# Performance work log

Hardware: AMD Instinct MI355X
Metric: run time of the kernel (lower is better)

## Reference

```python
import jax, jax.numpy as jnp
import numpy as np

B, L, H = 8, 2048, 1024
MASK_IDENTITY = True


def setup_inputs() -> dict:
    key = jax.random.key(0)
    ks = jax.random.split(key, 7)
    s = 1.0 / np.sqrt(H)
    return {
        "x": jax.random.normal(ks[0], (B, L, H), dtype=jnp.float32),
        "Wq": jax.random.uniform(ks[1], (H, H), jnp.float32, -s, s),
        "bq": jax.random.uniform(ks[2], (H,), jnp.float32, -s, s),
        "Wk": jax.random.uniform(ks[3], (H, H), jnp.float32, -s, s),
        "bk": jax.random.uniform(ks[4], (H,), jnp.float32, -s, s),
        "Wv": jax.random.uniform(ks[5], (H, H), jnp.float32, -s, s),
        "bv": jax.random.uniform(ks[6], (H,), jnp.float32, -s, s),
    }


def reference(x, Wq, bq, Wk, bk, Wv, bv):
    # Linear layers (torch Linear: y = x @ W.T + b)
    q = jnp.einsum("blh,oh->blo", x, Wq) + bq
    k = jnp.einsum("blh,oh->blo", x, Wk) + bk
    v = jnp.einsum("blh,oh->blo", x, Wv) + bv
    hidden = q.shape[-1]
    # NOTE: original scales by hidden_size, not sqrt(hidden_size)
    attn = jnp.einsum("blh,bmh->blm", q / hidden, k)  # [B, L, L]
    if MASK_IDENTITY:
        mask_value = -jnp.finfo(attn.dtype).max
        eye = jnp.eye(attn.shape[-1], dtype=bool)  # [L, L]
        attn = jnp.where(eye[None, :, :], mask_value, attn)
    attn = jax.nn.softmax(attn, axis=-1)
    return jnp.einsum("blm,bmh->blh", attn, v)
```

## Files before the change

### kernel.cpp

```cpp
#include <hip/hip_runtime.h>


typedef unsigned short u16;
typedef __bf16 bfx8 __attribute__((ext_vector_type(8)));
typedef float f32x4 __attribute__((ext_vector_type(4)));

__device__ __forceinline__ u16 f2bf(float f) {
    unsigned int x = __float_as_uint(f);
    unsigned int r = (x + 0x7fffu + ((x >> 16) & 1u)) >> 16;
    return (u16)r;
}
__device__ __forceinline__ float bf2f(u16 u) {
    return __uint_as_float(((unsigned int)u) << 16);
}

__global__ void f32_to_bf16(const float* __restrict__ src, u16* __restrict__ dst, int n8) {
    int i = blockIdx.x * blockDim.x + threadIdx.x;
    if (i < n8) {
        float4 a = ((const float4*)src)[i * 2];
        float4 b = ((const float4*)src)[i * 2 + 1];
        ushort4 lo; lo.x = f2bf(a.x); lo.y = f2bf(a.y); lo.z = f2bf(a.z); lo.w = f2bf(a.w);
        ushort4 hi; hi.x = f2bf(b.x); hi.y = f2bf(b.y); hi.z = f2bf(b.z); hi.w = f2bf(b.w);
        ((ushort4*)dst)[i * 2] = lo;
        ((ushort4*)dst)[i * 2 + 1] = hi;
    }
}

__global__ void transpose_bf16(const u16* __restrict__ src, u16* __restrict__ dst) {
    __shared__ u16 s[64][64 + 8];
    int z = blockIdx.z;
    int tm = blockIdx.x * 64;
    int th = blockIdx.y * 64;
    const u16* sp = src + (long)z * 2048 * 1024;
    u16* dp = dst + (long)z * 1024 * 2048;
    int t = threadIdx.x;
#pragma unroll
    for (int p = 0; p < 4; ++p) {
        int r = p * 16 + (t >> 4);
        int c = (t & 15) * 4;
        ushort4 v = *(const ushort4*)(sp + (long)(tm + r) * 1024 + th + c);
        s[r][c] = v.x; s[r][c + 1] = v.y; s[r][c + 2] = v.z; s[r][c + 3] = v.w;
    }
    __syncthreads();
#pragma unroll
    for (int p = 0; p < 4; ++p) {
        int hr = p * 16 + (t >> 4);
        int c = (t & 15) * 4;
        ushort4 v;
        v.x = s[c][hr]; v.y = s[c + 1][hr]; v.z = s[c + 2][hr]; v.w = s[c + 3][hr];
        *(ushort4*)(dp + (long)(th + hr) * 2048 + tm + c) = v;
    }
}

__global__ void row_sum(const u16* __restrict__ P, float* __restrict__ denom) {
    int row = blockIdx.x;
    int t = threadIdx.x;
    const u16* p = P + (long)row * 2048 + t * 8;
    ushort4 a = *(const ushort4*)p;
    ushort4 b = *(const ushort4*)(p + 4);
    float s = bf2f(a.x) + bf2f(a.y) + bf2f(a.z) + bf2f(a.w)
            + bf2f(b.x) + bf2f(b.y) + bf2f(b.z) + bf2f(b.w);
#pragma unroll
    for (int off = 32; off >= 1; off >>= 1) s += __shfl_down(s, off);
    __shared__ float ws[4];
    if ((t & 63) == 0) ws[t >> 6] = s;
    __syncthreads();
    if (t == 0) denom[row] = ws[0] + ws[1] + ws[2] + ws[3];
}

#define BM 128
#define BN 128
#define BK 64

template <int MODE>
__global__ __launch_bounds__(256, 2) void gemm_nt(
    const u16* __restrict__ Ab, const u16* __restrict__ Bb,
    int K, int lda, int ldb,
    long strideA, long strideB,
    const float* __restrict__ biasCat,
    u16* __restrict__ outBf, long strideP,
    const float* __restrict__ denom,
    float* __restrict__ outF)
{
    __shared__ __align__(16) u16 sA[2][BM * BK];
    __shared__ __align__(16) u16 sB[2][BN * BK];
    const int tid  = threadIdx.x;
    const int lane = tid & 63;
    const int wid  = tid >> 6;
    const int wr = wid >> 1, wc = wid & 1;
    const int z = blockIdx.z;
    const u16* A = Ab + (long)z * strideA + (long)blockIdx.x * BM * lda;
    const u16* B = Bb + (long)z * strideB + (long)blockIdx.y * BN * ldb;
    const int ldab = lda * 2, ldbb = ldb * 2;

    f32x4 acc[4][4] = {};
    const int nt = K / BK;

    auto stage = [&](int buf, int t) {
        const char* ga = (const char*)A + (long)t * (BK * 2);
        const char* gb = (const char*)B + (long)t * (BK * 2);
#pragma unroll
        for (int i = 0; i < 4; ++i) {
            int c  = i * 256 + tid;
            int r  = c >> 3;
            int lb = (c & 7) << 4;
            int sb = lb ^ ((r & 7) << 4);
            {
                const char* g = ga + (long)r * ldab + sb;
                char* l = (char*)&sA[buf][0] + (wid << 10) + (i << 12);
                __builtin_amdgcn_global_load_lds((__attribute__((address_space(1))) void*)g,
                                                 (__attribute__((address_space(3))) void*)l, 16, 0, 0);
            }
            {
                const char* g = gb + (long)r * ldbb + sb;
                char* l = (char*)&sB[buf][0] + (wid << 10) + (i << 12);
                __builtin_amdgcn_global_load_lds((__attribute__((address_space(1))) void*)g,
                                                 (__attribute__((address_space(3))) void*)l, 16, 0, 0);
            }
        }
    };

    stage(0, 0);
    __syncthreads();
    int cur = 0;
    for (int t = 0; t < nt; ++t) {
        if (t + 1 < nt) stage(cur ^ 1, t + 1);
#pragma unroll
        for (int kk = 0; kk < 2; ++kk) {
            bfx8 av[4], bv[4];
#pragma unroll
            for (int mi = 0; mi < 4; ++mi) {
                int row = wr * 64 + mi * 16 + (lane & 15);
                int kb  = kk * 64 + ((lane >> 4) << 4);
                int off = row * 128 + (kb ^ ((row & 7) << 4));
                av[mi] = *(const bfx8*)((const char*)&sA[cur][0] + off);
            }
#pragma unroll
            for (int ni = 0; ni < 4; ++ni) {
                int row = wc * 64 + ni * 16 + (lane & 15);
                int kb  = kk * 64 + ((lane >> 4) << 4);
                int off = row * 128 + (kb ^ ((row & 7) << 4));
                bv[ni] = *(const bfx8*)((const char*)&sB[cur][0] + off);
            }
#pragma unroll
            for (int mi = 0; mi < 4; ++mi)
#pragma unroll
                for (int ni = 0; ni < 4; ++ni)
                    acc[mi][ni] = __builtin_amdgcn_mfma_f32_16x16x32_bf16(av[mi], bv[ni], acc[mi][ni], 0, 0, 0);
        }
        __syncthreads();
        cur ^= 1;
    }

#pragma unroll
    for (int mi = 0; mi < 4; ++mi) {
#pragma unroll
        for (int ni = 0; ni < 4; ++ni) {
#pragma unroll
            for (int r = 0; r < 4; ++r) {
                int grow = blockIdx.x * BM + wr * 64 + mi * 16 + ((lane >> 4) << 2) + r;
                int gcol = blockIdx.y * BN + wc * 64 + ni * 16 + (lane & 15);
                float v = acc[mi][ni][r];
                if constexpr (MODE == 0) {
                    v += biasCat[gcol];
                    if (gcol < 1024) v *= (1.0f / 1024.0f);
                    int which = gcol >> 10;
                    long dst = (long)which * (16384L * 1024) + (long)grow * 1024 + (gcol & 1023);
                    outBf[dst] = f2bf(v);
                } else if constexpr (MODE == 1) {
                    float p = (grow == gcol) ? 0.0f : __expf(v);
                    outBf[(long)z * strideP + (long)grow * 2048 + gcol] = f2bf(p);
                } else {
                    float d = denom[z * 2048 + grow];
                    outF[(long)z * (2048L * 1024) + (long)grow * 1024 + gcol] = v / d;
                }
            }
        }
    }
}

extern "C" void kernel_launch(void* const* d_in, const int* in_sizes, int n_in,
                              void* d_out, int out_size, void* d_ws, size_t ws_size,
                              hipStream_t stream) {
    const float* x  = (const float*)d_in[0];
    const float* Wq = (const float*)d_in[1];
    const float* bq = (const float*)d_in[2];
    const float* Wk = (const float*)d_in[3];
    const float* bk = (const float*)d_in[4];
    const float* Wv = (const float*)d_in[5];
    const float* bv = (const float*)d_in[6];
    float* out = (float*)d_out;

    const long XB_OFF   = 0;
    const long WB_OFF   = 33554432;
    const long BIAS_OFF = WB_OFF + 6291456;
    const long DEN_OFF  = BIAS_OFF + 12288;
    const long QKV_OFF  = DEN_OFF + 65536;
    const long PB_OFF   = QKV_OFF + 2L * 33554432;
    const unsigned long long NEED = (unsigned long long)(PB_OFF + 67108864);
    if (ws_size < NEED) return;

    char* ws = (char*)d_ws;
    u16*   xb      = (u16*)(ws + XB_OFF);
    u16*   vT      = (u16*)(ws + XB_OFF);
    u16*   Wb      = (u16*)(ws + WB_OFF);
    float* biasCat = (float*)(ws + BIAS_OFF);
    float* den     = (float*)(ws + DEN_OFF);
    u16*   qkv     = (u16*)(ws + QKV_OFF);
    u16*   qb = qkv;
    u16*   kb = qkv + 16384L * 1024;
    u16*   vb = qkv + 2L * 16384 * 1024;
    u16*   Pb = (u16*)(ws + PB_OFF);

    f32_to_bf16<<<8192, 256, 0, stream>>>(x, xb, 2097152);
    f32_to_bf16<<<512, 256, 0, stream>>>(Wq, Wb, 131072);
    f32_to_bf16<<<512, 256, 0, stream>>>(Wk, Wb + 1048576, 131072);
    f32_to_bf16<<<512, 256, 0, stream>>>(Wv, Wb + 2097152, 131072);
    hipMemcpyAsync(biasCat,        bq, 4096, hipMemcpyDeviceToDevice, stream);
    hipMemcpyAsync(biasCat + 1024, bk, 4096, hipMemcpyDeviceToDevice, stream);
    hipMemcpyAsync(biasCat + 2048, bv, 4096, hipMemcpyDeviceToDevice, stream);

    gemm_nt<0><<<dim3(128, 24, 1), 256, 0, stream>>>(
        xb, Wb, 1024, 1024, 1024, 0, 0, biasCat, qkv, 0, nullptr, nullptr);

    transpose_bf16<<<dim3(32, 16, 8), 256, 0, stream>>>(vb, vT);

    gemm_nt<1><<<dim3(16, 16, 8), 256, 0, stream>>>(
        qb, kb, 1024, 1024, 1024, 2048L * 1024, 2048L * 1024,
        nullptr, Pb, 2048L * 2048, nullptr, nullptr);

    row_sum<<<16384, 256, 0, stream>>>(Pb, den);

    gemm_nt<2><<<dim3(16, 8, 8), 256, 0, stream>>>(
        Pb, vT, 2048, 2048, 2048, 2048L * 2048, 1024L * 2048,
        nullptr, nullptr, 0, den, out);
}
```

Baseline: 437.5 us.

## Use 256x256 8-wave GEMM with phased pipeline and fuse row sums

Replaces the 128x128 4-wave GEMM with a 256x256 tile, 512-thread kernel. The new kernel uses a four-phase main loop that interleaves LDS reads, global-to-LDS prefetch up to two k-steps ahead, barriers and setprio around MFMA clusters. The softmax denominator is now accumulated in the QK^T epilogue through shuffle reduction and atomicAdd, which removes the separate row_sum pass over P and needs a memset of den. The larger tiles raise data reuse but cut block counts (e.g. 256 blocks for the PV GEMM) and use 128KB LDS, which risks occupancy and SM fill.

```diff
diff --git a/kernel.cpp b/kernel.cpp
--- a/kernel.cpp
+++ b/kernel.cpp
@@ -52,128 +52,139 @@
     }
 }
 
-__global__ void row_sum(const u16* __restrict__ P, float* __restrict__ denom) {
-    int row = blockIdx.x;
-    int t = threadIdx.x;
-    const u16* p = P + (long)row * 2048 + t * 8;
-    ushort4 a = *(const ushort4*)p;
-    ushort4 b = *(const ushort4*)(p + 4);
-    float s = bf2f(a.x) + bf2f(a.y) + bf2f(a.z) + bf2f(a.w)
-            + bf2f(b.x) + bf2f(b.y) + bf2f(b.z) + bf2f(b.w);
-#pragma unroll
-    for (int off = 32; off >= 1; off >>= 1) s += __shfl_down(s, off);
-    __shared__ float ws[4];
-    if ((t & 63) == 0) ws[t >> 6] = s;
-    __syncthreads();
-    if (t == 0) denom[row] = ws[0] + ws[1] + ws[2] + ws[3];
-}
-
-#define BM 128
-#define BN 128
-#define BK 64
+
+#define PH_MID() do{ asm volatile("" ::: "memory"); __builtin_amdgcn_s_barrier(); \
+    asm volatile("s_waitcnt lgkmcnt(0)" ::: "memory"); __builtin_amdgcn_sched_barrier(0); \
+    __builtin_amdgcn_s_setprio(1); }while(0)
+#define PH_END() do{ __builtin_amdgcn_s_setprio(0); asm volatile("" ::: "memory"); \
+    __builtin_amdgcn_s_barrier(); }while(0)
+
+#define RD_A(cur, mibase) do{ \
+    const char* _b = smem + (cur)*65536 + (wr*128 + (mibase)*16 + rA)*128; \
+    a[0][0] = *(const bfx8*)(_b + 0*2048 + ofk0); a[0][1] = *(const bfx8*)(_b + 0*2048 + ofk1); \
+    a[1][0] = *(const bfx8*)(_b + 1*2048 + ofk0); a[1][1] = *(const bfx8*)(_b + 1*2048 + ofk1); \
+    a[2][0] = *(const bfx8*)(_b + 2*2048 + ofk0); a[2][1] = *(const bfx8*)(_b + 2*2048 + ofk1); \
+    a[3][0] = *(const bfx8*)(_b + 3*2048 + ofk0); a[3][1] = *(const bfx8*)(_b + 3*2048 + ofk1); \
+}while(0)
+
+#define RD_B(cur, nibase) do{ \
+    const char* _b = smem + (cur)*65536 + 32768 + (wc*64 + (nibase)*16 + rA)*128; \
+    b[(nibase)+0][0] = *(const bfx8*)(_b + 0*2048 + ofk0); b[(nibase)+0][1] = *(const bfx8*)(_b + 0*2048 + ofk1); \
+    b[(nibase)+1][0] = *(const bfx8*)(_b + 1*2048 + ofk0); b[(nibase)+1][1] = *(const bfx8*)(_b + 1*2048 + ofk1); \
+}while(0)
+
+#define MMQ(M0, N0) do{ \
+    _Pragma("unroll") \
+    for (int ks = 0; ks < 2; ++ks) \
+    _Pragma("unroll") \
+    for (int mi = 0; mi < 4; ++mi) \
+    _Pragma("unroll") \
+    for (int ni = 0; ni < 2; ++ni) \
+        acc[(M0)+mi][(N0)+ni] = __builtin_amdgcn_mfma_f32_16x16x32_bf16(a[mi][ks], b[(N0)+ni][ks], acc[(M0)+mi][(N0)+ni], 0, 0, 0); \
+}while(0)
 
 template <int MODE>
-__global__ __launch_bounds__(256, 2) void gemm_nt(
+__global__ __launch_bounds__(512, 2) void gemm8(
     const u16* __restrict__ Ab, const u16* __restrict__ Bb,
     int K, int lda, int ldb,
     long strideA, long strideB,
     const float* __restrict__ biasCat,
     u16* __restrict__ outBf, long strideP,
-    const float* __restrict__ denom,
+    float* __restrict__ den,
     float* __restrict__ outF)
 {
-    __shared__ __align__(16) u16 sA[2][BM * BK];
-    __shared__ __align__(16) u16 sB[2][BN * BK];
+    __shared__ __align__(16) char smem[131072];
     const int tid  = threadIdx.x;
     const int lane = tid & 63;
     const int wid  = tid >> 6;
-    const int wr = wid >> 1, wc = wid & 1;
+    const int wr = wid >> 2, wc = wid & 3;
     const int z = blockIdx.z;
-    const u16* A = Ab + (long)z * strideA + (long)blockIdx.x * BM * lda;
-    const u16* B = Bb + (long)z * strideB + (long)blockIdx.y * BN * ldb;
-    const int ldab = lda * 2, ldbb = ldb * 2;
-
-    f32x4 acc[4][4] = {};
-    const int nt = K / BK;
-
-    auto stage = [&](int buf, int t) {
-        const char* ga = (const char*)A + (long)t * (BK * 2);
-        const char* gb = (const char*)B + (long)t * (BK * 2);
-#pragma unroll
-        for (int i = 0; i < 4; ++i) {
-            int c  = i * 256 + tid;
-            int r  = c >> 3;
-            int lb = (c & 7) << 4;
-            int sb = lb ^ ((r & 7) << 4);
-            {
-                const char* g = ga + (long)r * ldab + sb;
-                char* l = (char*)&sA[buf][0] + (wid << 10) + (i << 12);
-                __builtin_amdgcn_global_load_lds((__attribute__((address_space(1))) void*)g,
-                                                 (__attribute__((address_space(3))) void*)l, 16, 0, 0);
-            }
-            {
-                const char* g = gb + (long)r * ldbb + sb;
-                char* l = (char*)&sB[buf][0] + (wid << 10) + (i << 12);
-                __builtin_amdgcn_global_load_lds((__attribute__((address_space(1))) void*)g,
-                                                 (__attribute__((address_space(3))) void*)l, 16, 0, 0);
-            }
+    const u16* A = Ab + (long)z * strideA + (long)blockIdx.x * 256 * lda;
+    const u16* B = Bb + (long)z * strideB + (long)blockIdx.y * 256 * ldb;
+    const int NT = K >> 6;
+
+    const int rA  = lane & 15;
+    const int cg  = lane >> 4;
+    const int swz = rA & 7;
+    const int ofk0 = ((cg)     ^ swz) << 4;
+    const int ofk1 = ((cg | 4) ^ swz) << 4;
+
+    f32x4 acc[8][4] = {};
+    bfx8 a[4][2], b[4][2];
+
+    auto stage = [&](int buf, int isB, int half, int t) {
+        const u16* src = isB ? B : A;
+        const int ld = isB ? ldb : lda;
+#pragma unroll
+        for (int rnd = 0; rnd < 2; ++rnd) {
+            int c = rnd * 512 + tid;
+            int row = half * 128 + (c >> 3);
+            int slot = c & 7;
+            const u16* g = src + (long)row * ld + t * 64 + ((slot ^ (row & 7)) << 3);
+            char* l = (char*)smem + buf * 65536 + isB * 32768 + half * 16384 + rnd * 8192 + wid * 1024;
+            __builtin_amdgcn_global_load_lds((__attribute__((address_space(1))) void*)g,
+                                             (__attribute__((address_space(3))) void*)l, 16, 0, 0);
         }
     };
 
-    stage(0, 0);
-    __syncthreads();
+    stage(0, 0, 0, 0); stage(0, 0, 1, 0); stage(0, 1, 0, 0); stage(0, 1, 1, 0);
+    stage(1, 1, 0, 1); stage(1, 1, 1, 1);
+    asm volatile("s_waitcnt vmcnt(4)" ::: "memory");
+    __builtin_amdgcn_s_barrier();
+
     int cur = 0;
-    for (int t = 0; t < nt; ++t) {
-        if (t + 1 < nt) stage(cur ^ 1, t + 1);
-#pragma unroll
-        for (int kk = 0; kk < 2; ++kk) {
-            bfx8 av[4], bv[4];
-#pragma unroll
-            for (int mi = 0; mi < 4; ++mi) {
-                int row = wr * 64 + mi * 16 + (lane & 15);
-                int kb  = kk * 64 + ((lane >> 4) << 4);
-                int off = row * 128 + (kb ^ ((row & 7) << 4));
-                av[mi] = *(const bfx8*)((const char*)&sA[cur][0] + off);
-            }
-#pragma unroll
-            for (int ni = 0; ni < 4; ++ni) {
-                int row = wc * 64 + ni * 16 + (lane & 15);
-                int kb  = kk * 64 + ((lane >> 4) << 4);
-                int off = row * 128 + (kb ^ ((row & 7) << 4));
-                bv[ni] = *(const bfx8*)((const char*)&sB[cur][0] + off);
-            }
-#pragma unroll
-            for (int mi = 0; mi < 4; ++mi)
-#pragma unroll
-                for (int ni = 0; ni < 4; ++ni)
-                    acc[mi][ni] = __builtin_amdgcn_mfma_f32_16x16x32_bf16(av[mi], bv[ni], acc[mi][ni], 0, 0, 0);
-        }
-        __syncthreads();
-        cur ^= 1;
-    }
-
-#pragma unroll
-    for (int mi = 0; mi < 4; ++mi) {
-#pragma unroll
-        for (int ni = 0; ni < 4; ++ni) {
-#pragma unroll
-            for (int r = 0; r < 4; ++r) {
-                int grow = blockIdx.x * BM + wr * 64 + mi * 16 + ((lane >> 4) << 2) + r;
-                int gcol = blockIdx.y * BN + wc * 64 + ni * 16 + (lane & 15);
-                float v = acc[mi][ni][r];
-                if constexpr (MODE == 0) {
-                    v += biasCat[gcol];
+    for (int t = 0; t < NT; ++t) {
+        const int nxt = cur ^ 1;
+        RD_A(cur, 0); RD_B(cur, 0);
+        if (t + 1 < NT) stage(nxt, 0, 0, t + 1);
+        PH_MID(); MMQ(0, 0); PH_END();
+        RD_B(cur, 2);
+        if (t + 1 < NT) stage(nxt, 0, 1, t + 1);
+        PH_MID(); MMQ(0, 2); PH_END();
+        RD_A(cur, 4);
+        if (t + 2 < NT) stage(cur, 1, 0, t + 2);
+        PH_MID(); MMQ(4, 2); PH_END();
+        if (t + 2 < NT) stage(cur, 1, 1, t + 2);
+        asm volatile("s_waitcnt vmcnt(4)" ::: "memory");
+        PH_MID(); MMQ(4, 0); PH_END();
+        cur = nxt;
+    }
+
+    const int r0 = blockIdx.x * 256 + wr * 128 + (cg << 2);
+    const int c0 = blockIdx.y * 256 + wc * 64 + rA;
+#pragma unroll
+    for (int mi = 0; mi < 8; ++mi) {
+#pragma unroll
+        for (int r = 0; r < 4; ++r) {
+            const int grow = r0 + mi * 16 + r;
+            if constexpr (MODE == 0) {
+#pragma unroll
+                for (int ni = 0; ni < 4; ++ni) {
+                    int gcol = c0 + ni * 16;
+                    float v = acc[mi][ni][r] + biasCat[gcol];
                     if (gcol < 1024) v *= (1.0f / 1024.0f);
                     int which = gcol >> 10;
                     long dst = (long)which * (16384L * 1024) + (long)grow * 1024 + (gcol & 1023);
                     outBf[dst] = f2bf(v);
-                } else if constexpr (MODE == 1) {
-                    float p = (grow == gcol) ? 0.0f : __expf(v);
-                    outBf[(long)z * strideP + (long)grow * 2048 + gcol] = f2bf(p);
-                } else {
-                    float d = denom[z * 2048 + grow];
-                    outF[(long)z * (2048L * 1024) + (long)grow * 1024 + gcol] = v / d;
                 }
+            } else if constexpr (MODE == 1) {
+                float s = 0.0f;
+#pragma unroll
+                for (int ni = 0; ni < 4; ++ni) {
+                    int gcol = c0 + ni * 16;
+                    float p = (grow == gcol) ? 0.0f : __expf(acc[mi][ni][r]);
+                    u16 pb = f2bf(p);
+                    outBf[(long)z * strideP + (long)grow * 2048 + gcol] = pb;
+                    s += bf2f(pb);
+                }
+                s += __shfl_xor(s, 1); s += __shfl_xor(s, 2);
+                s += __shfl_xor(s, 4); s += __shfl_xor(s, 8);
+                if (rA == 0) atomicAdd(&den[z * 2048 + grow], s);
+            } else {
+                float d = den[z * 2048 + grow];
+#pragma unroll
+                for (int ni = 0; ni < 4; ++ni)
+                    outF[(long)z * (2048L * 1024) + (long)grow * 1024 + (c0 + ni * 16)] = acc[mi][ni][r] / d;
             }
         }
     }
@@ -219,19 +230,18 @@
     hipMemcpyAsync(biasCat,        bq, 4096, hipMemcpyDeviceToDevice, stream);
     hipMemcpyAsync(biasCat + 1024, bk, 4096, hipMemcpyDeviceToDevice, stream);
     hipMemcpyAsync(biasCat + 2048, bv, 4096, hipMemcpyDeviceToDevice, stream);
-
-    gemm_nt<0><<<dim3(128, 24, 1), 256, 0, stream>>>(
+    hipMemsetAsync(den, 0, 65536, stream);
+
+    gemm8<0><<<dim3(64, 12, 1), 512, 0, stream>>>(
         xb, Wb, 1024, 1024, 1024, 0, 0, biasCat, qkv, 0, nullptr, nullptr);
 
     transpose_bf16<<<dim3(32, 16, 8), 256, 0, stream>>>(vb, vT);
 
-    gemm_nt<1><<<dim3(16, 16, 8), 256, 0, stream>>>(
+    gemm8<1><<<dim3(8, 8, 8), 512, 0, stream>>>(
         qb, kb, 1024, 1024, 1024, 2048L * 1024, 2048L * 1024,
-        nullptr, Pb, 2048L * 2048, nullptr, nullptr);
-
-    row_sum<<<16384, 256, 0, stream>>>(Pb, den);
-
-    gemm_nt<2><<<dim3(16, 8, 8), 256, 0, stream>>>(
+        nullptr, Pb, 2048L * 2048, den, nullptr);
+
+    gemm8<2><<<dim3(8, 4, 8), 512, 0, stream>>>(
         Pb, vT, 2048, 2048, 2048, 2048L * 2048, 1024L * 2048,
         nullptr, nullptr, 0, den, out);
 }
```

Result: faster. 389.2 us (-11.0%).
